# Optimization experiments

Hardware: AMD Instinct MI355X
Metric: run time of the kernel (lower is better)

## Reference

```python
import jax, jax.numpy as jnp
import numpy as np

N_NODES = 100000
N_EDGES = 800000
N_GRAPHS = 2000
VOCAB = 30000
EMB = 64
REL = 16
HID = 128
NCLASS = 10


def setup_inputs() -> dict:
    key = jax.random.key(0)
    ks = jax.random.split(key, 16)
    x_tokens = jax.random.randint(ks[0], (N_NODES,), 0, VOCAB)
    edge_index = jax.random.randint(ks[1], (2, N_EDGES), 0, N_NODES)
    edge_type = jax.random.randint(ks[2], (N_EDGES,), 0, 3)
    batch = jnp.sort(jax.random.randint(ks[3], (N_NODES,), 0, N_GRAPHS))
    s = lambda k, shp, fan: jax.random.normal(k, shp, jnp.float32) * (1.0 / np.sqrt(fan))
    return {
        "x_tokens": x_tokens,
        "edge_index": edge_index,
        "edge_type": edge_type,
        "batch": batch,
        "num_graphs": N_GRAPHS,
        "emb_table": s(ks[4], (VOCAB, EMB), EMB),
        "rel_table": s(ks[5], (3, REL), REL),
        "w1_l": s(ks[6], (EMB + REL, HID), EMB + REL),
        "b1": jnp.zeros((HID,), jnp.float32),
        "w1_r": s(ks[7], (EMB, HID), EMB),
        "w2_l": s(ks[8], (HID, HID), HID),
        "b2": jnp.zeros((HID,), jnp.float32),
        "w2_r": s(ks[9], (HID, HID), HID),
        "lin_w": s(ks[10], (HID, NCLASS), HID),
        "lin_b": jnp.zeros((NCLASS,), jnp.float32),
    }


def _mean_agg(msgs, dst, n_nodes):
    # segment-mean of per-edge messages into destination nodes
    summed = jax.ops.segment_sum(msgs, dst, num_segments=n_nodes)
    deg = jax.ops.segment_sum(jnp.ones((msgs.shape[0],), msgs.dtype), dst, num_segments=n_nodes)
    return summed / jnp.maximum(deg, 1.0)[:, None]


def reference(x_tokens, edge_index, edge_type, batch, num_graphs,
              emb_table, rel_table, w1_l, b1, w1_r, w2_l, b2, w2_r, lin_w, lin_b):
    n_nodes = x_tokens.shape[0]
    src, dst = edge_index[0], edge_index[1]
    x = emb_table[x_tokens]                                  # [N, 64]
    rel_e = rel_table[edge_type]                             # [E, 16]
    src_feat = jnp.concatenate([x[src], rel_e], axis=1)      # [E, 80]
    # SAGEConv 1: mean-aggregate relation-aware messages + root transform
    agg1 = _mean_agg(src_feat, dst, n_nodes)                 # [N, 80]
    h = agg1 @ w1_l + b1 + x @ w1_r                          # [N, 128]
    h = jax.nn.relu(h)
    # SAGEConv 2
    agg2 = _mean_agg(h[src], dst, n_nodes)                   # [N, 128]
    h2 = agg2 @ w2_l + b2 + h @ w2_r                         # [N, 128]
    # global max pool over graphs, then ReLU -> (dropout: eval identity) -> Linear
    g = jax.ops.segment_max(h2, batch, num_segments=num_graphs)  # [G, 128]
    g = jax.nn.relu(g)
    return g @ lin_w + lin_b                                 # [G, nclass]
```

## Files before the change

### kernel.cpp

```cpp
#include <hip/hip_runtime.h>
#include <hip/hip_bf16.h>

#define NN 100000
#define NE 800000
#define NG 2000
#define EMB 64
#define HID 128
#define NCLS 10

#define NBKT 196
#define EPB 4096
#define NBA ((NE + EPB - 1) / EPB)

typedef __attribute__((ext_vector_type(8))) short short8;
typedef __attribute__((ext_vector_type(4))) float f32x4;
typedef unsigned short u16;
typedef unsigned int u32;

static __device__ __forceinline__ unsigned fenc(float f) {
    unsigned u = __float_as_uint(f);
    return (u & 0x80000000u) ? ~u : (u | 0x80000000u);
}
static __device__ __forceinline__ float fdec(unsigned u) {
    return (u & 0x80000000u) ? __uint_as_float(u & 0x7FFFFFFFu) : __uint_as_float(~u);
}
static __device__ __forceinline__ u16 f2bf(float f) {
    u32 u = __float_as_uint(f);
    return (u16)((u + 0x7FFFu + ((u >> 16) & 1u)) >> 16);
}

__global__ __launch_bounds__(256) void k_pre(
    const int* __restrict__ tok, const float* __restrict__ emb,
    const int* __restrict__ dst, int* __restrict__ counts,
    unsigned* __restrict__ genc, float* __restrict__ relp,
    u16* __restrict__ Bt1, u16* __restrict__ Bt2,
    const float* __restrict__ rel_table, const float* __restrict__ w1l,
    const float* __restrict__ w1r, const float* __restrict__ w2l,
    const float* __restrict__ w2r, u32* __restrict__ axw) {
    __shared__ int hist[NBKT];
    int g = blockIdx.x, t = threadIdx.x;
    if (g < NBA) {
        for (int i = t; i < NBKT; i += 256) hist[i] = 0;
        __syncthreads();
        int base = g * EPB;
        for (int j = t; j < EPB; j += 256) {
            int e = base + j;
            if (e < NE) atomicAdd(&hist[dst[e] >> 9], 1);
        }
        __syncthreads();
        for (int i = t; i < NBKT; i += 256)
            counts[i * NBA + g] = hist[i];
        return;
    }
    int i = (g - NBA) * 256 + t;
    {
        int n = i >> 5, p = i & 31;
        float2 e = *(const float2*)&emb[tok[n] * EMB + p * 2];
        axw[n * 64 + 32 + p] = (u32)f2bf(e.x) | ((u32)f2bf(e.y) << 16);
    }
    if (i < NG * HID) genc[i] = 0x007FFFFFu;
    if (i < 3 * HID) {
        int tt = i >> 7, j = i & 127;
        float s = 0.f;
        for (int k = 0; k < 16; ++k)
            s += rel_table[tt * 16 + k] * w1l[(64 + k) * HID + j];
        relp[i] = s;
    }
    if (i < 128 * 128) {
        int c = i >> 7, k = i & 127;
        float w = (k < 64) ? w1l[k * HID + c] : w1r[(k - 64) * HID + c];
        Bt1[c * 128 + k] = f2bf(w);
    }
    if (i < 128 * 256) {
        int c = i >> 8, k = i & 255;
        float w = (k < 128) ? w2l[k * HID + c] : w2r[(k - 128) * HID + c];
        Bt2[c * 256 + k] = f2bf(w);
    }
}

__global__ __launch_bounds__(256) void kS1(const int* __restrict__ counts,
                                           int* __restrict__ scanned,
                                           int* __restrict__ bucketT) {
    __shared__ int s[256];
    int b = blockIdx.x, t = threadIdx.x;
    int v = (t < NBA) ? counts[b * NBA + t] : 0;
    s[t] = v;
    __syncthreads();
    for (int off = 1; off < 256; off <<= 1) {
        int u = (t >= off) ? s[t - off] : 0;
        __syncthreads();
        s[t] += u;
        __syncthreads();
    }
    if (t < NBA) scanned[b * NBA + t] = s[t] - v;
    if (t == 255) bucketT[b] = s[255];
}

__global__ __launch_bounds__(256) void k_part(const int* __restrict__ src,
                                              const int* __restrict__ dst,
                                              const int* __restrict__ et,
                                              const int* __restrict__ scanned,
                                              const int* __restrict__ bucketT,
                                              u32* __restrict__ coarse) {
    __shared__ int cur[NBKT];
    __shared__ int s[256];
    int t = threadIdx.x;
    int v = (t < NBKT) ? bucketT[t] : 0;
    s[t] = v;
    __syncthreads();
    for (int off = 1; off < 256; off <<= 1) {
        int u = (t >= off) ? s[t - off] : 0;
        __syncthreads();
        s[t] += u;
        __syncthreads();
    }
    if (t < NBKT) cur[t] = (s[t] - v) + scanned[t * NBA + blockIdx.x];
    __syncthreads();
    int b0 = blockIdx.x * EPB;
    for (int j = t; j < EPB; j += 256) {
        int e = b0 + j;
        if (e < NE) {
            int d = dst[e];
            int pos = atomicAdd(&cur[d >> 9], 1);
            coarse[pos] = (u32)src[e] | ((u32)et[e] << 17) | ((u32)(d & 511) << 19);
        }
    }
}

__global__ __launch_bounds__(256) void k_csr(const int* __restrict__ bucketT,
                                             const u32* __restrict__ coarse,
                                             int* __restrict__ offsets,
                                             int* __restrict__ packed) {
    __shared__ int hist[512];
    __shared__ int ex[512];
    __shared__ int ts[256];
    __shared__ int sBeg, sEnd;
    int b = blockIdx.x, t = threadIdx.x;
    {
        int v = (t < NBKT) ? bucketT[t] : 0;
        ts[t] = v;
        __syncthreads();
        for (int off = 1; off < 256; off <<= 1) {
            int u = (t >= off) ? ts[t - off] : 0;
            __syncthreads();
            ts[t] += u;
            __syncthreads();
        }
        if (t == b) { sBeg = ts[b] - v; sEnd = ts[b]; }
        __syncthreads();
    }
    int beg = sBeg, end = sEnd;
    hist[t] = 0; hist[t + 256] = 0;
    __syncthreads();
    for (int i = beg + t; i < end; i += 256)
        atomicAdd(&hist[(coarse[i] >> 19) & 511], 1);
    __syncthreads();
    int a0 = hist[2 * t], a1 = hist[2 * t + 1];
    int sum = a0 + a1;
    ts[t] = sum;
    __syncthreads();
    for (int off = 1; off < 256; off <<= 1) {
        int u = (t >= off) ? ts[t - off] : 0;
        __syncthreads();
        ts[t] += u;
        __syncthreads();
    }
    int ep = ts[t] - sum;
    ex[2 * t] = ep;
    ex[2 * t + 1] = ep + a0;
    __syncthreads();
    int node0 = b * 512;
    if (node0 + 2 * t < NN)     offsets[node0 + 2 * t]     = beg + ex[2 * t];
    if (node0 + 2 * t + 1 < NN) offsets[node0 + 2 * t + 1] = beg + ex[2 * t + 1];
    if (b == NBKT - 1 && t == 0) offsets[NN] = NE;
    hist[2 * t] = beg + ex[2 * t];
    hist[2 * t + 1] = beg + ex[2 * t + 1];
    __syncthreads();
    for (int i = beg + t; i < end; i += 256) {
        u32 pk = coarse[i];
        int pos = atomicAdd(&hist[(pk >> 19) & 511], 1);
        packed[pos] = (int)(pk & 0x1FFFFu) | (int)(((pk >> 17) & 3u) << 20);
    }
}

__global__ __launch_bounds__(256) void k_agg1(
    const int* __restrict__ offsets, const int* __restrict__ packed,
    u32* __restrict__ axw, float* __restrict__ fc) {
    int node = (blockIdx.x * 256 + threadIdx.x) >> 6;
    int lane = threadIdx.x & 63;
    int half = lane >> 5;
    int fl = lane & 31;
    int beg = offsets[node], end = offsets[node + 1];
    float a0 = 0.f, a1 = 0.f;
    int c0 = 0, c1 = 0, c2 = 0;
    for (int cb = beg; cb < end; cb += 64) {
        int pk = packed[min(cb + lane, NE - 1)];
        int cnt = min(end - cb, 64);
        int j = 0;
        for (; j + 8 <= cnt; j += 8) {
            #pragma unroll
            for (int q = 0; q < 4; ++q) {
                int p = __shfl(pk, j + q * 2 + half, 64);
                u32 v = axw[(p & 0xFFFFF) * 64 + 32 + fl];
                a0 += __uint_as_float(v << 16);
                a1 += __uint_as_float(v & 0xFFFF0000u);
                int t = p >> 20;
                c0 += (t == 0); c1 += (t == 1); c2 += (t == 2);
            }
        }
        for (; j < cnt; j += 2) {
            int idx = j + half;
            if (idx < cnt) {
                int p = __shfl(pk, idx, 64);
                u32 v = axw[(p & 0xFFFFF) * 64 + 32 + fl];
                a0 += __uint_as_float(v << 16);
                a1 += __uint_as_float(v & 0xFFFF0000u);
                int t = p >> 20;
                c0 += (t == 0); c1 += (t == 1); c2 += (t == 2);
            }
        }
    }
    a0 += __shfl_xor(a0, 32, 64);
    a1 += __shfl_xor(a1, 32, 64);
    c0 += __shfl_xor(c0, 32, 64);
    c1 += __shfl_xor(c1, 32, 64);
    c2 += __shfl_xor(c2, 32, 64);
    float inv = 1.0f / (float)max(end - beg, 1);
    if (half == 0)
        axw[node * 64 + fl] = (u32)f2bf(a0 * inv) | ((u32)f2bf(a1 * inv) << 16);
    if (lane == 0)
        *(float4*)&fc[node * 4] = make_float4(c0 * inv, c1 * inv, c2 * inv, 0.f);
}

__global__ __launch_bounds__(256) void k_agg2(
    const int* __restrict__ offsets, const int* __restrict__ packed,
    u32* __restrict__ ahw) {
    int node = (blockIdx.x * 256 + threadIdx.x) >> 6;
    int lane = threadIdx.x & 63;
    int beg = offsets[node], end = offsets[node + 1];
    float a0 = 0.f, a1 = 0.f;
    for (int cb = beg; cb < end; cb += 64) {
        int pk = packed[min(cb + lane, NE - 1)] & 0xFFFFF;
        int cnt = min(end - cb, 64);
        int j = 0;
        for (; j + 4 <= cnt; j += 4) {
            int s0 = __shfl(pk, j, 64), s1 = __shfl(pk, j + 1, 64);
            int s2 = __shfl(pk, j + 2, 64), s3 = __shfl(pk, j + 3, 64);
            u32 u0 = ahw[(size_t)s0 * 128 + 64 + lane];
            u32 u1 = ahw[(size_t)s1 * 128 + 64 + lane];
            u32 u2 = ahw[(size_t)s2 * 128 + 64 + lane];
            u32 u3 = ahw[(size_t)s3 * 128 + 64 + lane];
            a0 += __uint_as_float(u0 << 16) + __uint_as_float(u1 << 16)
                + __uint_as_float(u2 << 16) + __uint_as_float(u3 << 16);
            a1 += __uint_as_float(u0 & 0xFFFF0000u) + __uint_as_float(u1 & 0xFFFF0000u)
                + __uint_as_float(u2 & 0xFFFF0000u) + __uint_as_float(u3 & 0xFFFF0000u);
        }
        for (; j < cnt; ++j) {
            u32 u = ahw[(size_t)__shfl(pk, j, 64) * 128 + 64 + lane];
            a0 += __uint_as_float(u << 16);
            a1 += __uint_as_float(u & 0xFFFF0000u);
        }
    }
    float inv = 1.0f / (float)max(end - beg, 1);
    ahw[node * 128 + lane] = (u32)f2bf(a0 * inv) | ((u32)f2bf(a1 * inv) << 16);
}

__global__ __launch_bounds__(512) void k_gemm1(
    const u16* __restrict__ ax, const float* __restrict__ fc,
    const u16* __restrict__ Bt1, const float* __restrict__ b1,
    const float* __restrict__ relp, u16* __restrict__ ah) {
    __shared__ u16 Bs[128 * 128];
    int tid = threadIdx.x;
    int lane = tid & 63, w = tid >> 6;
    int mbase = blockIdx.x * 128;
    int r16 = lane & 15;
    int kg = (lane >> 4) * 8;
    int r = min(mbase + w * 16 + r16, NN - 1);
    short8 a[4];
    #pragma unroll
    for (int s = 0; s < 4; ++s)
        a[s] = *(const short8*)(ax + (size_t)r * 128 + s * 32 + kg);
    for (int i = tid; i < 2048; i += 512) {
        int col = i >> 4, p = i & 15;
        ((short8*)Bs)[i] = *(const short8*)(Bt1 + col * 128 + ((p ^ (col & 7)) << 3));
    }
    __syncthreads();
    f32x4 acc[8] = {};
    #pragma unroll
    for (int s = 0; s < 4; ++s) {
        int c = s * 4 + (lane >> 4);
        #pragma unroll
        for (int nf = 0; nf < 8; ++nf) {
            int col = nf * 16 + r16;
            short8 b = ((const short8*)Bs)[col * 16 + (c ^ (col & 7))];
            acc[nf] = __builtin_amdgcn_mfma_f32_16x16x32_bf16(a[s], b, acc[nf], 0, 0, 0);
        }
    }
    #pragma unroll
    for (int reg = 0; reg < 4; ++reg) {
        int row = mbase + w * 16 + (lane >> 4) * 4 + reg;
        if (row >= NN) continue;
        float4 f = *(const float4*)&fc[row * 4];
        #pragma unroll
        for (int nf = 0; nf < 8; ++nf) {
            int cc = nf * 16 + r16;
            float v = acc[nf][reg] + b1[cc]
                    + f.x * relp[cc] + f.y * relp[128 + cc] + f.z * relp[256 + cc];
            ah[(size_t)row * 256 + 128 + cc] = f2bf(fmaxf(v, 0.f));
        }
    }
}

__global__ __launch_bounds__(512) void k_gemm2(
    const u16* __restrict__ ah, const u16* __restrict__ Bt2,
    const float* __restrict__ b2, const int* __restrict__ batch,
    unsigned* __restrict__ genc) {
    __shared__ u16 Bs[128 * 256];
    int tid = threadIdx.x;
    int lane = tid & 63, w = tid >> 6;
    int mbase = blockIdx.x * 128;
    int r16 = lane & 15;
    int kg = (lane >> 4) * 8;
    int r = min(mbase + w * 16 + r16, NN - 1);
    short8 a[8];
    #pragma unroll
    for (int s = 0; s < 8; ++s)
        a[s] = *(const short8*)(ah + (size_t)r * 256 + s * 32 + kg);
    for (int i = tid; i < 4096; i += 512) {
        int col = i >> 5, p = i & 31;
        ((short8*)Bs)[i] = *(const short8*)(Bt2 + col * 256 + ((p ^ (col & 7)) << 3));
    }
    __syncthreads();
    f32x4 acc[8] = {};
    #pragma unroll
    for (int s = 0; s < 8; ++s) {
        int c = s * 4 + (lane >> 4);
        #pragma unroll
        for (int nf = 0; nf < 8; ++nf) {
            int col = nf * 16 + r16;
            short8 b = ((const short8*)Bs)[col * 32 + (c ^ (col & 7))];
            acc[nf] = __builtin_amdgcn_mfma_f32_16x16x32_bf16(a[s], b, acc[nf], 0, 0, 0);
        }
    }
    float bv[8];
    #pragma unroll
    for (int nf = 0; nf < 8; ++nf) bv[nf] = b2[nf * 16 + r16];
    int wbeg = mbase + w * 16;
    if (wbeg >= NN) return;
    int wlast = min(wbeg + 15, NN - 1);
    if (batch[wbeg] == batch[wlast]) {
        int bt = batch[wbeg];
        float vm[8];
        #pragma unroll
        for (int nf = 0; nf < 8; ++nf) {
            f32x4 v4 = acc[nf];
            vm[nf] = fmaxf(fmaxf(v4[0], v4[1]), fmaxf(v4[2], v4[3]));
        }
        #pragma unroll
        for (int nf = 0; nf < 8; ++nf)
            vm[nf] = fmaxf(vm[nf], __shfl_xor(vm[nf], 16, 64));
        #pragma unroll
        for (int nf = 0; nf < 8; ++nf)
            vm[nf] = fmaxf(vm[nf], __shfl_xor(vm[nf], 32, 64));
        if ((lane >> 4) == 0) {
            #pragma unroll
            for (int nf = 0; nf < 8; ++nf)
                atomicMax(&genc[bt * HID + nf * 16 + r16], fenc(vm[nf] + bv[nf]));
        }
    } else {
        int r0 = wbeg + (lane >> 4) * 4;
        if (r0 < NN) {
            if (r0 + 3 < NN && batch[r0] == batch[r0 + 3]) {
                int bt = batch[r0];
                #pragma unroll
                for (int nf = 0; nf < 8; ++nf) {
                    int cc = nf * 16 + r16;
                    f32x4 v4 = acc[nf];
                    float v = fmaxf(fmaxf(v4[0], v4[1]), fmaxf(v4[2], v4[3])) + bv[nf];
                    atomicMax(&genc[bt * HID + cc], fenc(v));
                }
            } else {
                #pragma unroll
                for (int reg = 0; reg < 4; ++reg) {
                    int row = r0 + reg;
                    if (row >= NN) continue;
                    int bt = batch[row];
                    #pragma unroll
                    for (int nf = 0; nf < 8; ++nf) {
                        int cc = nf * 16 + r16;
                        atomicMax(&genc[bt * HID + cc], fenc(acc[nf][reg] + bv[nf]));
                    }
                }
            }
        }
    }
}

__global__ void k_final(const unsigned* __restrict__ genc,
                        const float* __restrict__ lin_w, const float* __restrict__ lin_b,
                        float* __restrict__ out) {
    int gr = blockIdx.x;
    int lane = threadIdx.x;
    float g0 = fmaxf(fdec(genc[gr * HID + lane]), 0.f);
    float g1 = fmaxf(fdec(genc[gr * HID + 64 + lane]), 0.f);
    #pragma unroll
    for (int c = 0; c < NCLS; ++c) {
        float p = g0 * lin_w[lane * NCLS + c] + g1 * lin_w[(lane + 64) * NCLS + c];
        for (int off = 32; off > 0; off >>= 1)
            p += __shfl_down(p, off, 64);
        if (lane == 0) out[gr * NCLS + c] = p + lin_b[c];
    }
}

extern "C" void kernel_launch(void* const* d_in, const int* in_sizes, int n_in,
                              void* d_out, int out_size, void* d_ws, size_t ws_size,
                              hipStream_t stream) {
    const int* x_tokens   = (const int*)d_in[0];
    const int* edge_index = (const int*)d_in[1];
    const int* edge_type  = (const int*)d_in[2];
    const int* batch      = (const int*)d_in[3];
    const float* emb_table = (const float*)d_in[5];
    const float* rel_table = (const float*)d_in[6];
    const float* w1_l = (const float*)d_in[7];
    const float* b1   = (const float*)d_in[8];
    const float* w1_r = (const float*)d_in[9];
    const float* w2_l = (const float*)d_in[10];
    const float* b2   = (const float*)d_in[11];
    const float* w2_r = (const float*)d_in[12];
    const float* lin_w = (const float*)d_in[13];
    const float* lin_b = (const float*)d_in[14];
    float* out = (float*)d_out;

    const int* src = edge_index;
    const int* dst = edge_index + NE;

    char* ws = (char*)d_ws;
    size_t off = 0;
    auto alloc = [&](size_t bytes) {
        void* p = ws + off;
        off = (off + bytes + 255) & ~(size_t)255;
        return p;
    };
    u16* ax      = (u16*)alloc((size_t)NN * 128 * 2);
    u16* ah      = (u16*)alloc((size_t)NN * 256 * 2);
    float* fc    = (float*)alloc((size_t)NN * 4 * 4);
    int* offsets = (int*)alloc((size_t)(NN + 1) * 4);
    int* packed  = (int*)alloc((size_t)NE * 4);
    u32* coarse  = (u32*)alloc((size_t)NE * 4);
    int* counts  = (int*)alloc((size_t)NBKT * NBA * 4);
    int* scanned = (int*)alloc((size_t)NBKT * NBA * 4);
    int* bucketT = (int*)alloc((size_t)NBKT * 4);
    unsigned* genc = (unsigned*)alloc((size_t)NG * HID * 4);
    float* relp  = (float*)alloc((size_t)3 * HID * 4);
    u16* Bt1     = (u16*)alloc((size_t)128 * 128 * 2);
    u16* Bt2     = (u16*)alloc((size_t)128 * 256 * 2);
    (void)ws_size; (void)in_sizes; (void)n_in; (void)out_size;

    const int MT = (NN + 127) / 128;
    const int PRE = NBA + NN * 32 / 256;

    hipLaunchKernelGGL(k_pre,   dim3(PRE), dim3(256), 0, stream,
                       x_tokens, emb_table, dst, counts, genc, relp, Bt1, Bt2,
                       rel_table, w1_l, w1_r, w2_l, w2_r, (u32*)ax);
    hipLaunchKernelGGL(kS1,     dim3(NBKT), dim3(256), 0, stream, counts, scanned, bucketT);
    hipLaunchKernelGGL(k_part,  dim3(NBA), dim3(256), 0, stream,
                       src, dst, edge_type, scanned, bucketT, coarse);
    hipLaunchKernelGGL(k_csr,   dim3(NBKT), dim3(256), 0, stream,
                       bucketT, coarse, offsets, packed);
    hipLaunchKernelGGL(k_agg1,  dim3(NN / 4), dim3(256), 0, stream,
                       offsets, packed, (u32*)ax, fc);
    hipLaunchKernelGGL(k_gemm1, dim3(MT), dim3(512), 0, stream,
                       ax, fc, Bt1, b1, relp, ah);
    hipLaunchKernelGGL(k_agg2,  dim3(NN / 4), dim3(256), 0, stream,
                       offsets, packed, (u32*)ah);
    hipLaunchKernelGGL(k_gemm2, dim3(MT), dim3(512), 0, stream,
                       ah, Bt2, b2, batch, genc);
    hipLaunchKernelGGL(k_final, dim3(NG), dim3(64), 0, stream, genc, lin_w, lin_b, out);
}
```

Measured before the change: 166.3 us.

## Use half-wave per node with 8-byte gathers in aggregation; halve gemm2 LDS tile

The aggregation kernels now give each node 32 lanes instead of 64. Each lane gathers a uint2 (8 bytes) per neighbour row and keeps four accumulators, so every wave handles two nodes at once. This is meant to cut per-node lane waste and issue overhead on the gather-bound scatter-mean, since the average degree is about 8. Separately, k_gemm2 loads its B matrix into shared memory in two 128-column K halves with an extra sync, halving LDS use to raise occupancy at the cost of a second load phase.

```diff
diff --git a/kernel.cpp b/kernel.cpp
--- a/kernel.cpp
+++ b/kernel.cpp
@@ -186,83 +186,103 @@
 __global__ __launch_bounds__(256) void k_agg1(
     const int* __restrict__ offsets, const int* __restrict__ packed,
     u32* __restrict__ axw, float* __restrict__ fc) {
-    int node = (blockIdx.x * 256 + threadIdx.x) >> 6;
-    int lane = threadIdx.x & 63;
-    int half = lane >> 5;
-    int fl = lane & 31;
+    int node = (blockIdx.x * 256 + threadIdx.x) >> 5;
+    int gl = threadIdx.x & 31;
+    int sub = gl >> 4;
+    int sl = gl & 15;
     int beg = offsets[node], end = offsets[node + 1];
-    float a0 = 0.f, a1 = 0.f;
+    float a0 = 0.f, a1 = 0.f, a2 = 0.f, a3 = 0.f;
     int c0 = 0, c1 = 0, c2 = 0;
-    for (int cb = beg; cb < end; cb += 64) {
-        int pk = packed[min(cb + lane, NE - 1)];
-        int cnt = min(end - cb, 64);
+    for (int cb = beg; cb < end; cb += 32) {
+        int pk = packed[min(cb + gl, NE - 1)];
+        int cnt = min(end - cb, 32);
         int j = 0;
         for (; j + 8 <= cnt; j += 8) {
             #pragma unroll
             for (int q = 0; q < 4; ++q) {
-                int p = __shfl(pk, j + q * 2 + half, 64);
-                u32 v = axw[(p & 0xFFFFF) * 64 + 32 + fl];
-                a0 += __uint_as_float(v << 16);
-                a1 += __uint_as_float(v & 0xFFFF0000u);
+                int p = __shfl(pk, j + q * 2 + sub, 32);
+                uint2 v = *(const uint2*)&axw[(p & 0xFFFFF) * 64 + 32 + 2 * sl];
+                a0 += __uint_as_float(v.x << 16);
+                a1 += __uint_as_float(v.x & 0xFFFF0000u);
+                a2 += __uint_as_float(v.y << 16);
+                a3 += __uint_as_float(v.y & 0xFFFF0000u);
                 int t = p >> 20;
                 c0 += (t == 0); c1 += (t == 1); c2 += (t == 2);
             }
         }
         for (; j < cnt; j += 2) {
-            int idx = j + half;
+            int idx = j + sub;
             if (idx < cnt) {
-                int p = __shfl(pk, idx, 64);
-                u32 v = axw[(p & 0xFFFFF) * 64 + 32 + fl];
-                a0 += __uint_as_float(v << 16);
-                a1 += __uint_as_float(v & 0xFFFF0000u);
+                int p = __shfl(pk, idx, 32);
+                uint2 v = *(const uint2*)&axw[(p & 0xFFFFF) * 64 + 32 + 2 * sl];
+                a0 += __uint_as_float(v.x << 16);
+                a1 += __uint_as_float(v.x & 0xFFFF0000u);
+                a2 += __uint_as_float(v.y << 16);
+                a3 += __uint_as_float(v.y & 0xFFFF0000u);
                 int t = p >> 20;
                 c0 += (t == 0); c1 += (t == 1); c2 += (t == 2);
             }
         }
     }
-    a0 += __shfl_xor(a0, 32, 64);
-    a1 += __shfl_xor(a1, 32, 64);
-    c0 += __shfl_xor(c0, 32, 64);
-    c1 += __shfl_xor(c1, 32, 64);
-    c2 += __shfl_xor(c2, 32, 64);
+    a0 += __shfl_xor(a0, 16, 32);
+    a1 += __shfl_xor(a1, 16, 32);
+    a2 += __shfl_xor(a2, 16, 32);
+    a3 += __shfl_xor(a3, 16, 32);
+    c0 += __shfl_xor(c0, 16, 32);
+    c1 += __shfl_xor(c1, 16, 32);
+    c2 += __shfl_xor(c2, 16, 32);
     float inv = 1.0f / (float)max(end - beg, 1);
-    if (half == 0)
-        axw[node * 64 + fl] = (u32)f2bf(a0 * inv) | ((u32)f2bf(a1 * inv) << 16);
-    if (lane == 0)
+    if (sub == 0) {
+        uint2 o;
+        o.x = (u32)f2bf(a0 * inv) | ((u32)f2bf(a1 * inv) << 16);
+        o.y = (u32)f2bf(a2 * inv) | ((u32)f2bf(a3 * inv) << 16);
+        *(uint2*)&axw[node * 64 + 2 * sl] = o;
+    }
+    if (gl == 0)
         *(float4*)&fc[node * 4] = make_float4(c0 * inv, c1 * inv, c2 * inv, 0.f);
 }
 
 __global__ __launch_bounds__(256) void k_agg2(
     const int* __restrict__ offsets, const int* __restrict__ packed,
     u32* __restrict__ ahw) {
-    int node = (blockIdx.x * 256 + threadIdx.x) >> 6;
-    int lane = threadIdx.x & 63;
+    int node = (blockIdx.x * 256 + threadIdx.x) >> 5;
+    int gl = threadIdx.x & 31;
     int beg = offsets[node], end = offsets[node + 1];
-    float a0 = 0.f, a1 = 0.f;
-    for (int cb = beg; cb < end; cb += 64) {
-        int pk = packed[min(cb + lane, NE - 1)] & 0xFFFFF;
-        int cnt = min(end - cb, 64);
+    float a0 = 0.f, a1 = 0.f, a2 = 0.f, a3 = 0.f;
+    for (int cb = beg; cb < end; cb += 32) {
+        int pk = packed[min(cb + gl, NE - 1)] & 0xFFFFF;
+        int cnt = min(end - cb, 32);
         int j = 0;
         for (; j + 4 <= cnt; j += 4) {
-            int s0 = __shfl(pk, j, 64), s1 = __shfl(pk, j + 1, 64);
-            int s2 = __shfl(pk, j + 2, 64), s3 = __shfl(pk, j + 3, 64);
-            u32 u0 = ahw[(size_t)s0 * 128 + 64 + lane];
-            u32 u1 = ahw[(size_t)s1 * 128 + 64 + lane];
-            u32 u2 = ahw[(size_t)s2 * 128 + 64 + lane];
-            u32 u3 = ahw[(size_t)s3 * 128 + 64 + lane];
-            a0 += __uint_as_float(u0 << 16) + __uint_as_float(u1 << 16)
-                + __uint_as_float(u2 << 16) + __uint_as_float(u3 << 16);
-            a1 += __uint_as_float(u0 & 0xFFFF0000u) + __uint_as_float(u1 & 0xFFFF0000u)
-                + __uint_as_float(u2 & 0xFFFF0000u) + __uint_as_float(u3 & 0xFFFF0000u);
+            int s0 = __shfl(pk, j, 32), s1 = __shfl(pk, j + 1, 32);
+            int s2 = __shfl(pk, j + 2, 32), s3 = __shfl(pk, j + 3, 32);
+            uint2 v0 = *(const uint2*)&ahw[(size_t)s0 * 128 + 64 + 2 * gl];
+            uint2 v1 = *(const uint2*)&ahw[(size_t)s1 * 128 + 64 + 2 * gl];
+            uint2 v2 = *(const uint2*)&ahw[(size_t)s2 * 128 + 64 + 2 * gl];
+            uint2 v3 = *(const uint2*)&ahw[(size_t)s3 * 128 + 64 + 2 * gl];
+            a0 += __uint_as_float(v0.x << 16) + __uint_as_float(v1.x << 16)
+                + __uint_as_float(v2.x << 16) + __uint_as_float(v3.x << 16);
+            a1 += __uint_as_float(v0.x & 0xFFFF0000u) + __uint_as_float(v1.x & 0xFFFF0000u)
+                + __uint_as_float(v2.x & 0xFFFF0000u) + __uint_as_float(v3.x & 0xFFFF0000u);
+            a2 += __uint_as_float(v0.y << 16) + __uint_as_float(v1.y << 16)
+                + __uint_as_float(v2.y << 16) + __uint_as_float(v3.y << 16);
+            a3 += __uint_as_float(v0.y & 0xFFFF0000u) + __uint_as_float(v1.y & 0xFFFF0000u)
+                + __uint_as_float(v2.y & 0xFFFF0000u) + __uint_as_float(v3.y & 0xFFFF0000u);
         }
         for (; j < cnt; ++j) {
-            u32 u = ahw[(size_t)__shfl(pk, j, 64) * 128 + 64 + lane];
-            a0 += __uint_as_float(u << 16);
-            a1 += __uint_as_float(u & 0xFFFF0000u);
+            int p = __shfl(pk, j, 32);
+            uint2 v = *(const uint2*)&ahw[(size_t)p * 128 + 64 + 2 * gl];
+            a0 += __uint_as_float(v.x << 16);
+            a1 += __uint_as_float(v.x & 0xFFFF0000u);
+            a2 += __uint_as_float(v.y << 16);
+            a3 += __uint_as_float(v.y & 0xFFFF0000u);
         }
     }
     float inv = 1.0f / (float)max(end - beg, 1);
-    ahw[node * 128 + lane] = (u32)f2bf(a0 * inv) | ((u32)f2bf(a1 * inv) << 16);
+    uint2 o;
+    o.x = (u32)f2bf(a0 * inv) | ((u32)f2bf(a1 * inv) << 16);
+    o.y = (u32)f2bf(a2 * inv) | ((u32)f2bf(a3 * inv) << 16);
+    *(uint2*)&ahw[node * 128 + 2 * gl] = o;
 }
 
 __global__ __launch_bounds__(512) void k_gemm1(
@@ -315,7 +335,7 @@
     const u16* __restrict__ ah, const u16* __restrict__ Bt2,
     const float* __restrict__ b2, const int* __restrict__ batch,
     unsigned* __restrict__ genc) {
-    __shared__ u16 Bs[128 * 256];
+    __shared__ u16 Bs[128 * 128];
     int tid = threadIdx.x;
     int lane = tid & 63, w = tid >> 6;
     int mbase = blockIdx.x * 128;
@@ -326,19 +346,35 @@
     #pragma unroll
     for (int s = 0; s < 8; ++s)
         a[s] = *(const short8*)(ah + (size_t)r * 256 + s * 32 + kg);
-    for (int i = tid; i < 4096; i += 512) {
-        int col = i >> 5, p = i & 31;
+    for (int i = tid; i < 2048; i += 512) {
+        int col = i >> 4, p = i & 15;
         ((short8*)Bs)[i] = *(const short8*)(Bt2 + col * 256 + ((p ^ (col & 7)) << 3));
     }
     __syncthreads();
     f32x4 acc[8] = {};
     #pragma unroll
-    for (int s = 0; s < 8; ++s) {
+    for (int s = 0; s < 4; ++s) {
         int c = s * 4 + (lane >> 4);
         #pragma unroll
         for (int nf = 0; nf < 8; ++nf) {
             int col = nf * 16 + r16;
-            short8 b = ((const short8*)Bs)[col * 32 + (c ^ (col & 7))];
+            short8 b = ((const short8*)Bs)[col * 16 + (c ^ (col & 7))];
+            acc[nf] = __builtin_amdgcn_mfma_f32_16x16x32_bf16(a[s], b, acc[nf], 0, 0, 0);
+        }
+    }
+    __syncthreads();
+    for (int i = tid; i < 2048; i += 512) {
+        int col = i >> 4, p = i & 15;
+        ((short8*)Bs)[i] = *(const short8*)(Bt2 + col * 256 + 128 + ((p ^ (col & 7)) << 3));
+    }
+    __syncthreads();
+    #pragma unroll
+    for (int s = 4; s < 8; ++s) {
+        int c = (s - 4) * 4 + (lane >> 4);
+        #pragma unroll
+        for (int nf = 0; nf < 8; ++nf) {
+            int col = nf * 16 + r16;
+            short8 b = ((const short8*)Bs)[col * 16 + (c ^ (col & 7))];
             acc[nf] = __builtin_amdgcn_mfma_f32_16x16x32_bf16(a[s], b, acc[nf], 0, 0, 0);
         }
     }
@@ -458,6 +494,7 @@
 
     const int MT = (NN + 127) / 128;
     const int PRE = NBA + NN * 32 / 256;
+    const int AGG = NN / 8;
 
     hipLaunchKernelGGL(k_pre,   dim3(PRE), dim3(256), 0, stream,
                        x_tokens, emb_table, dst, counts, genc, relp, Bt1, Bt2,
@@ -467,11 +504,11 @@
                        src, dst, edge_type, scanned, bucketT, coarse);
     hipLaunchKernelGGL(k_csr,   dim3(NBKT), dim3(256), 0, stream,
                        bucketT, coarse, offsets, packed);
-    hipLaunchKernelGGL(k_agg1,  dim3(NN / 4), dim3(256), 0, stream,
+    hipLaunchKernelGGL(k_agg1,  dim3(AGG), dim3(256), 0, stream,
                        offsets, packed, (u32*)ax, fc);
     hipLaunchKernelGGL(k_gemm1, dim3(MT), dim3(512), 0, stream,
                        ax, fc, Bt1, b1, relp, ah);
-    hipLaunchKernelGGL(k_agg2,  dim3(NN / 4), dim3(256), 0, stream,
+    hipLaunchKernelGGL(k_agg2,  dim3(AGG), dim3(256), 0, stream,
                        offsets, packed, (u32*)ah);
     hipLaunchKernelGGL(k_gemm2, dim3(MT), dim3(512), 0, stream,
                        ah, Bt2, b2, batch, genc);
```

New measurement: 154.2 us. 1.08x faster.
